# Performance work log

Hardware: AMD Instinct MI355X
Metric: run time of the kernel (lower is better)

The kernel has to match this reference:

```python
import jax, jax.numpy as jnp
import numpy as np

EPS = 1e-4
B, C_IN, H, W = 64, 512, 14, 14
P, NCLS = 2000, 200


def setup_inputs() -> dict:
    key = jax.random.key(0)
    k1, k2 = jax.random.split(key)
    x = jax.random.normal(k1, (B, C_IN, H, W), dtype=jnp.float32)
    prototype_vectors = jax.random.uniform(k2, (P, C_IN, 1, 1), dtype=jnp.float32)
    # fc weight init: +1 for the prototype's own class, -0.5 otherwise
    per_class = P // NCLS
    assoc = (np.arange(P) // per_class)[:, None] == np.arange(NCLS)[None, :]  # [P, NCLS]
    assoc = assoc.astype(np.float32)
    fc_weight = jnp.asarray(1.0 * assoc.T - 0.5 * (1.0 - assoc.T))  # [NCLS, P]
    return {"x": x, "prototype_vectors": prototype_vectors, "fc_weight": fc_weight}


def reference(x, prototype_vectors, fc_weight):
    # prototypes are 1x1, so the conv is a channel contraction
    p = prototype_vectors[:, :, 0, 0]  # [P, C]
    xp = jnp.einsum('bchw,pc->bphw', x, p)                 # cross term
    x2_patch_sum = jnp.sum(x * x, axis=1, keepdims=True)   # [B,1,H,W] (ones-kernel conv, identical across P)
    p2 = jnp.sum(p * p, axis=1)[None, :, None, None]       # [1,P,1,1]
    dists = jax.nn.relu(x2_patch_sum - 2.0 * xp + p2)      # [B,P,H,W]
    min_dists = jnp.min(dists, axis=(2, 3))                # global min-pool -> [B,P]
    activations = jnp.log((min_dists + 1.0) / (min_dists + EPS))
    logits = activations @ fc_weight.T                     # [B,NCLS]
    return (x, min_dists, dists, activations, logits)
```

## Files before the change

### kernel.cpp

```cpp
#include <hip/hip_runtime.h>
#include <math.h>


#define EPSV 1e-4f
typedef unsigned short ushort_t;

constexpr int NB  = 64;
constexpr int NC  = 512;
constexpr int NHW = 196;
constexpr int NP  = 2000;
constexpr int NPAD = 2048;
constexpr int NCL = 200;
constexpr int MM   = NB * NHW;
constexpr int XTOT = NB * NC * NHW;

constexpr long long OFF_MIN = XTOT;
constexpr long long OFF_D   = OFF_MIN + (long long)NB * NP;
constexpr long long OFF_ACT = OFF_D + (long long)NB * NP * NHW;
constexpr long long OFF_LOG = OFF_ACT + (long long)NB * NP;

typedef __attribute__((ext_vector_type(8))) short short8;
typedef __attribute__((ext_vector_type(4))) float f32x4;

__device__ __forceinline__ void bsplit(float f, unsigned& h, unsigned& l) {
    unsigned u = __float_as_uint(f);
    h = (u + 0x7FFFu + ((u >> 16) & 1u)) >> 16;
    float fl = f - __uint_as_float(h << 16);
    unsigned u2 = __float_as_uint(fl);
    l = (u2 + 0x7FFFu + ((u2 >> 16) & 1u)) >> 16;
}

__device__ __forceinline__ void gl_lds16(const void* g, void* l) {
    __builtin_amdgcn_global_load_lds(
        (const __attribute__((address_space(1))) unsigned int*)g,
        (__attribute__((address_space(3))) unsigned int*)l, 16, 0, 0);
}

__global__ void fill_kernel(float* __restrict__ mind, float* __restrict__ x2) {
    int i = blockIdx.x * 256 + threadIdx.x;
    if (i < NB * NP) mind[i] = 3.402823466e38f;
    if (i < MM)      x2[i] = 0.f;
}

__global__ __launch_bounds__(256) void splitx_kernel(const float* __restrict__ x,
                                                     ushort_t* __restrict__ xh,
                                                     ushort_t* __restrict__ xl,
                                                     float* __restrict__ x2) {
    __shared__ float tl[64 * 197];
    const int b = blockIdx.x >> 3, cc = blockIdx.x & 7;
    const int c0 = cc * 64;
    const float* src = x + ((size_t)b * NC + c0) * NHW;
    for (int idx = threadIdx.x; idx < 64 * 196; idx += 256) {
        int cl = idx / 196, hw = idx - cl * 196;
        tl[cl * 197 + hw] = src[idx];
    }
    __syncthreads();
    for (int idx = threadIdx.x; idx < 64 * 196; idx += 256) {
        int hw = idx >> 6, cl = idx & 63;
        float v = tl[cl * 197 + hw];
        unsigned h, l; bsplit(v, h, l);
        size_t o = ((size_t)(b * 196 + hw)) * NC + c0 + cl;
        xh[o] = (ushort_t)h;
        xl[o] = (ushort_t)l;
    }
    if (threadIdx.x < 196) {
        float s = 0.f;
        #pragma unroll 8
        for (int cl = 0; cl < 64; ++cl) { float v = tl[cl * 197 + threadIdx.x]; s += v * v; }
        atomicAdd(&x2[b * 196 + threadIdx.x], s);
    }
}

__global__ void splitp_kernel(const float* __restrict__ proto,
                              ushort_t* __restrict__ ph, ushort_t* __restrict__ pl,
                              float* __restrict__ p2) {
    int p = blockIdx.x * 4 + (threadIdx.x >> 6);
    int l = threadIdx.x & 63;
    unsigned hs[8], ls[8];
    float s = 0.f;
    if (p < NP) {
        const float4* pr = (const float4*)(proto + (size_t)p * NC + l * 8);
        float4 a = pr[0], bb = pr[1];
        float vv[8] = {a.x, a.y, a.z, a.w, bb.x, bb.y, bb.z, bb.w};
        #pragma unroll
        for (int k = 0; k < 8; ++k) { bsplit(vv[k], hs[k], ls[k]); s += vv[k] * vv[k]; }
    } else {
        #pragma unroll
        for (int k = 0; k < 8; ++k) { hs[k] = 0; ls[k] = 0; }
    }
    uint4 H = make_uint4(hs[0] | (hs[1] << 16), hs[2] | (hs[3] << 16),
                         hs[4] | (hs[5] << 16), hs[6] | (hs[7] << 16));
    uint4 L = make_uint4(ls[0] | (ls[1] << 16), ls[2] | (ls[3] << 16),
                         ls[4] | (ls[5] << 16), ls[6] | (ls[7] << 16));
    *(uint4*)&ph[(size_t)p * NC + l * 8] = H;
    *(uint4*)&pl[(size_t)p * NC + l * 8] = L;
    for (int off = 32; off; off >>= 1) s += __shfl_down(s, off, 64);
    if (l == 0) p2[p] = s;
}

__global__ __launch_bounds__(256) void gemm_kernel(
    const ushort_t* __restrict__ xh, const ushort_t* __restrict__ xl,
    const ushort_t* __restrict__ ph, const ushort_t* __restrict__ pl,
    const float* __restrict__ p2, const float* __restrict__ x2,
    float* __restrict__ dists, unsigned* __restrict__ mind)
{
    __shared__ ushort_t Ah[128 * 32];
    __shared__ ushort_t Al[128 * 32];
    __shared__ ushort_t Bh[128 * 32];
    __shared__ ushort_t Bl[128 * 32];

    const int wg  = blockIdx.x;
    const int swz = (wg & 7) * 196 + (wg >> 3);
    const int nt  = swz / 98, mt = swz - nt * 98;

    const int t = threadIdx.x;
    const int lane = t & 63, lm = lane & 15, kg = lane >> 4;
    const int w = t >> 6, wp = w >> 1, wx = w & 1;

    const size_t ga = (size_t)(mt * 128 + (t >> 2)) * NC + (t & 3) * 8;
    const size_t gb = (size_t)(nt * 128 + (t >> 2)) * NC + (t & 3) * 8;
    const size_t gs = (size_t)64 * NC;

    f32x4 acc[4][4];
    #pragma unroll
    for (int i = 0; i < 4; ++i)
        #pragma unroll
        for (int j = 0; j < 4; ++j) acc[i][j] = 0.f;

    for (int c0 = 0; c0 < NC; c0 += 32) {
        gl_lds16(xh + ga + c0,      &Ah[t * 8]);
        gl_lds16(xh + ga + gs + c0, &Ah[2048 + t * 8]);
        gl_lds16(xl + ga + c0,      &Al[t * 8]);
        gl_lds16(xl + ga + gs + c0, &Al[2048 + t * 8]);
        gl_lds16(ph + gb + c0,      &Bh[t * 8]);
        gl_lds16(ph + gb + gs + c0, &Bh[2048 + t * 8]);
        gl_lds16(pl + gb + c0,      &Bl[t * 8]);
        gl_lds16(pl + gb + gs + c0, &Bl[2048 + t * 8]);
        __syncthreads();

        short8 PH[4], PL[4], XH[4], XL[4];
        #pragma unroll
        for (int i = 0; i < 4; ++i) {
            PH[i] = *(const short8*)&Bh[(wp * 64 + i * 16 + lm) * 32 + kg * 8];
            PL[i] = *(const short8*)&Bl[(wp * 64 + i * 16 + lm) * 32 + kg * 8];
            XH[i] = *(const short8*)&Ah[(wx * 64 + i * 16 + lm) * 32 + kg * 8];
            XL[i] = *(const short8*)&Al[(wx * 64 + i * 16 + lm) * 32 + kg * 8];
        }
        #pragma unroll
        for (int i = 0; i < 4; ++i)
            #pragma unroll
            for (int j = 0; j < 4; ++j) {
                acc[i][j] = __builtin_amdgcn_mfma_f32_16x16x32_bf16(PH[i], XH[j], acc[i][j], 0, 0, 0);
                acc[i][j] = __builtin_amdgcn_mfma_f32_16x16x32_bf16(PL[i], XH[j], acc[i][j], 0, 0, 0);
                acc[i][j] = __builtin_amdgcn_mfma_f32_16x16x32_bf16(PH[i], XL[j], acc[i][j], 0, 0, 0);
            }
        __syncthreads();
    }

    const int mhalf = mt * 128 + wx * 64;
    const int b0h = mhalf / 196;
    const int b1h = (mhalf + 63) / 196;
    float x2v[4]; int bj[4]; size_t dbase[4];
    #pragma unroll
    for (int j = 0; j < 4; ++j) {
        int m = mhalf + j * 16 + lm;
        x2v[j] = x2[m];
        int b = m / 196, hw = m - b * 196;
        bj[j] = b;
        dbase[j] = (size_t)b * ((size_t)NP * NHW) + hw;
    }
    #pragma unroll
    for (int i = 0; i < 4; ++i) {
        #pragma unroll
        for (int r = 0; r < 4; ++r) {
            int p = nt * 128 + wp * 64 + i * 16 + kg * 4 + r;
            if (p < NP) {
                float p2v = p2[p];
                float mn0 = 3.402823466e38f, mn1 = 3.402823466e38f;
                #pragma unroll
                for (int j = 0; j < 4; ++j) {
                    float v = fmaxf(x2v[j] - 2.f * acc[i][j][r] + p2v, 0.f);
                    dists[dbase[j] + (size_t)p * NHW] = v;
                    if (bj[j] == b0h) mn0 = fminf(mn0, v); else mn1 = fminf(mn1, v);
                }
                #pragma unroll
                for (int off = 1; off < 16; off <<= 1) {
                    mn0 = fminf(mn0, __shfl_xor(mn0, off, 64));
                    mn1 = fminf(mn1, __shfl_xor(mn1, off, 64));
                }
                if (lm == 0) {
                    atomicMin(&mind[b0h * NP + p], __float_as_uint(mn0));
                    if (b1h != b0h) atomicMin(&mind[b1h * NP + p], __float_as_uint(mn1));
                }
            }
        }
    }
}

__global__ void act_kernel(const float* __restrict__ mind, float* __restrict__ act) {
    int i = blockIdx.x * 256 + threadIdx.x;
    if (i < NB * NP) { float md = mind[i]; act[i] = logf((md + 1.f) / (md + EPSV)); }
}

__global__ void logits_kernel(const float* __restrict__ act,
                              const float* __restrict__ fc, float* __restrict__ out) {
    int r = blockIdx.x * 4 + (threadIdx.x >> 6);
    int l = threadIdx.x & 63;
    int b = r / NCL, n = r - b * NCL;
    const float* arow = act + b * NP;
    const float* frow = fc + n * NP;
    float s = 0.f;
    for (int k = l; k < NP; k += 64) s += arow[k] * frow[k];
    for (int off = 32; off; off >>= 1) s += __shfl_down(s, off, 64);
    if (l == 0) out[r] = s;
}

__global__ void copy_kernel(const float4* __restrict__ in, float4* __restrict__ out, int n4) {
    for (int i = blockIdx.x * blockDim.x + threadIdx.x; i < n4; i += gridDim.x * blockDim.x)
        out[i] = in[i];
}

extern "C" void kernel_launch(void* const* d_in, const int* in_sizes, int n_in,
                              void* d_out, int out_size, void* d_ws, size_t ws_size,
                              hipStream_t stream) {
    const float* x     = (const float*)d_in[0];
    const float* proto = (const float*)d_in[1];
    const float* fc    = (const float*)d_in[2];
    float* out = (float*)d_out;

    ushort_t* xh = (ushort_t*)out;
    ushort_t* xl = xh + XTOT;
    ushort_t* ph = (ushort_t*)d_ws;
    ushort_t* pl = ph + (size_t)NPAD * NC;
    float*    p2 = (float*)(pl + (size_t)NPAD * NC);
    float*    x2 = p2 + NPAD;

    float* mind  = out + OFF_MIN;
    float* dists = out + OFF_D;
    float* act   = out + OFF_ACT;
    float* logit = out + OFF_LOG;

    fill_kernel<<<500, 256, 0, stream>>>(mind, x2);
    splitx_kernel<<<512, 256, 0, stream>>>(x, xh, xl, x2);
    splitp_kernel<<<512, 256, 0, stream>>>(proto, ph, pl, p2);

    gemm_kernel<<<1568, 256, 0, stream>>>(xh, xl, ph, pl, p2, x2, dists, (unsigned*)mind);

    act_kernel<<<500, 256, 0, stream>>>(mind, act);
    logits_kernel<<<3200, 256, 0, stream>>>(act, fc, logit);

    copy_kernel<<<2048, 256, 0, stream>>>((const float4*)x, (float4*)out, XTOT / 4);
}
```

Before: 305.2 us.

## Drop bf16 hi/lo split to single bf16 GEMM with swizzled LDS and nontemporal stores

Replaces the three-MFMA bf16x3 split-precision scheme with a single bf16 product, removing the low-part arrays, their conversion and their loads. The K tile grows to 64 with an XOR-swizzled LDS layout to avoid bank conflicts. The fill kernel is fused into the prototype split kernel, vectorised packed stores are used in splitx, and dists and the copy use nontemporal loads and stores. Plain bf16 loses precision in the cross term, which could break tolerance for distances near zero.

```diff
diff --git a/kernel.cpp b/kernel.cpp
--- a/kernel.cpp
+++ b/kernel.cpp
@@ -22,12 +22,9 @@
 typedef __attribute__((ext_vector_type(8))) short short8;
 typedef __attribute__((ext_vector_type(4))) float f32x4;
 
-__device__ __forceinline__ void bsplit(float f, unsigned& h, unsigned& l) {
+__device__ __forceinline__ unsigned bf16rne(float f) {
     unsigned u = __float_as_uint(f);
-    h = (u + 0x7FFFu + ((u >> 16) & 1u)) >> 16;
-    float fl = f - __uint_as_float(h << 16);
-    unsigned u2 = __float_as_uint(fl);
-    l = (u2 + 0x7FFFu + ((u2 >> 16) & 1u)) >> 16;
+    return (u + 0x7FFFu + ((u >> 16) & 1u)) >> 16;
 }
 
 __device__ __forceinline__ void gl_lds16(const void* g, void* l) {
@@ -36,32 +33,55 @@
         (__attribute__((address_space(3))) unsigned int*)l, 16, 0, 0);
 }
 
-__global__ void fill_kernel(float* __restrict__ mind, float* __restrict__ x2) {
-    int i = blockIdx.x * 256 + threadIdx.x;
-    if (i < NB * NP) mind[i] = 3.402823466e38f;
-    if (i < MM)      x2[i] = 0.f;
+__global__ __launch_bounds__(256) void splitp_kernel(const float* __restrict__ proto,
+                              ushort_t* __restrict__ ph, float* __restrict__ p2,
+                              float* __restrict__ mind, float* __restrict__ x2) {
+    int gi = blockIdx.x * 256 + threadIdx.x;
+    if (gi < NB * NP) mind[gi] = 3.402823466e38f;
+    if (gi < MM)      x2[gi]  = 0.f;
+
+    int p = blockIdx.x * 4 + (threadIdx.x >> 6);
+    int l = threadIdx.x & 63;
+    unsigned hs[8];
+    float s = 0.f;
+    if (p < NP) {
+        const float4* pr = (const float4*)(proto + (size_t)p * NC + l * 8);
+        float4 a = pr[0], bb = pr[1];
+        float vv[8] = {a.x, a.y, a.z, a.w, bb.x, bb.y, bb.z, bb.w};
+        #pragma unroll
+        for (int k = 0; k < 8; ++k) { hs[k] = bf16rne(vv[k]); s += vv[k] * vv[k]; }
+    } else {
+        #pragma unroll
+        for (int k = 0; k < 8; ++k) hs[k] = 0;
+    }
+    uint4 H = make_uint4(hs[0] | (hs[1] << 16), hs[2] | (hs[3] << 16),
+                         hs[4] | (hs[5] << 16), hs[6] | (hs[7] << 16));
+    int col = (l >> 3) * 64 + (((l & 7) ^ (p & 7)) << 3);
+    *(uint4*)&ph[(size_t)p * NC + col] = H;
+    for (int off = 32; off; off >>= 1) s += __shfl_down(s, off, 64);
+    if (l == 0) p2[p] = s;
 }
 
 __global__ __launch_bounds__(256) void splitx_kernel(const float* __restrict__ x,
                                                      ushort_t* __restrict__ xh,
-                                                     ushort_t* __restrict__ xl,
                                                      float* __restrict__ x2) {
     __shared__ float tl[64 * 197];
     const int b = blockIdx.x >> 3, cc = blockIdx.x & 7;
     const int c0 = cc * 64;
     const float* src = x + ((size_t)b * NC + c0) * NHW;
-    for (int idx = threadIdx.x; idx < 64 * 196; idx += 256) {
-        int cl = idx / 196, hw = idx - cl * 196;
-        tl[cl * 197 + hw] = src[idx];
-    }
+    for (int idx = threadIdx.x; idx < 64 * 196; idx += 256)
+        tl[(idx / 196) * 197 + (idx % 196)] = src[idx];
     __syncthreads();
-    for (int idx = threadIdx.x; idx < 64 * 196; idx += 256) {
-        int hw = idx >> 6, cl = idx & 63;
-        float v = tl[cl * 197 + hw];
-        unsigned h, l; bsplit(v, h, l);
-        size_t o = ((size_t)(b * 196 + hw)) * NC + c0 + cl;
-        xh[o] = (ushort_t)h;
-        xl[o] = (ushort_t)l;
+    for (int idx = threadIdx.x; idx < 1568; idx += 256) {
+        int hw = idx >> 3, slot = idx & 7;
+        int m = b * 196 + hw;
+        unsigned hs[8];
+        #pragma unroll
+        for (int e = 0; e < 8; ++e)
+            hs[e] = bf16rne(tl[(slot * 8 + e) * 197 + hw]);
+        uint4 H = make_uint4(hs[0] | (hs[1] << 16), hs[2] | (hs[3] << 16),
+                             hs[4] | (hs[5] << 16), hs[6] | (hs[7] << 16));
+        *(uint4*)&xh[(size_t)m * NC + c0 + ((slot ^ (m & 7)) << 3)] = H;
     }
     if (threadIdx.x < 196) {
         float s = 0.f;
@@ -71,43 +91,13 @@
     }
 }
 
-__global__ void splitp_kernel(const float* __restrict__ proto,
-                              ushort_t* __restrict__ ph, ushort_t* __restrict__ pl,
-                              float* __restrict__ p2) {
-    int p = blockIdx.x * 4 + (threadIdx.x >> 6);
-    int l = threadIdx.x & 63;
-    unsigned hs[8], ls[8];
-    float s = 0.f;
-    if (p < NP) {
-        const float4* pr = (const float4*)(proto + (size_t)p * NC + l * 8);
-        float4 a = pr[0], bb = pr[1];
-        float vv[8] = {a.x, a.y, a.z, a.w, bb.x, bb.y, bb.z, bb.w};
-        #pragma unroll
-        for (int k = 0; k < 8; ++k) { bsplit(vv[k], hs[k], ls[k]); s += vv[k] * vv[k]; }
-    } else {
-        #pragma unroll
-        for (int k = 0; k < 8; ++k) { hs[k] = 0; ls[k] = 0; }
-    }
-    uint4 H = make_uint4(hs[0] | (hs[1] << 16), hs[2] | (hs[3] << 16),
-                         hs[4] | (hs[5] << 16), hs[6] | (hs[7] << 16));
-    uint4 L = make_uint4(ls[0] | (ls[1] << 16), ls[2] | (ls[3] << 16),
-                         ls[4] | (ls[5] << 16), ls[6] | (ls[7] << 16));
-    *(uint4*)&ph[(size_t)p * NC + l * 8] = H;
-    *(uint4*)&pl[(size_t)p * NC + l * 8] = L;
-    for (int off = 32; off; off >>= 1) s += __shfl_down(s, off, 64);
-    if (l == 0) p2[p] = s;
-}
-
 __global__ __launch_bounds__(256) void gemm_kernel(
-    const ushort_t* __restrict__ xh, const ushort_t* __restrict__ xl,
-    const ushort_t* __restrict__ ph, const ushort_t* __restrict__ pl,
+    const ushort_t* __restrict__ xh, const ushort_t* __restrict__ ph,
     const float* __restrict__ p2, const float* __restrict__ x2,
     float* __restrict__ dists, unsigned* __restrict__ mind)
 {
-    __shared__ ushort_t Ah[128 * 32];
-    __shared__ ushort_t Al[128 * 32];
-    __shared__ ushort_t Bh[128 * 32];
-    __shared__ ushort_t Bl[128 * 32];
+    __shared__ ushort_t Ah[128 * 64];
+    __shared__ ushort_t Bh[128 * 64];
 
     const int wg  = blockIdx.x;
     const int swz = (wg & 7) * 196 + (wg >> 3);
@@ -117,9 +107,9 @@
     const int lane = t & 63, lm = lane & 15, kg = lane >> 4;
     const int w = t >> 6, wp = w >> 1, wx = w & 1;
 
-    const size_t ga = (size_t)(mt * 128 + (t >> 2)) * NC + (t & 3) * 8;
-    const size_t gb = (size_t)(nt * 128 + (t >> 2)) * NC + (t & 3) * 8;
-    const size_t gs = (size_t)64 * NC;
+    const size_t ga = (size_t)(mt * 128 + (t >> 3)) * NC + (t & 7) * 8;
+    const size_t gb = (size_t)(nt * 128 + (t >> 3)) * NC + (t & 7) * 8;
+    const size_t gs = (size_t)32 * NC;
 
     f32x4 acc[4][4];
     #pragma unroll
@@ -127,33 +117,33 @@
         #pragma unroll
         for (int j = 0; j < 4; ++j) acc[i][j] = 0.f;
 
-    for (int c0 = 0; c0 < NC; c0 += 32) {
-        gl_lds16(xh + ga + c0,      &Ah[t * 8]);
-        gl_lds16(xh + ga + gs + c0, &Ah[2048 + t * 8]);
-        gl_lds16(xl + ga + c0,      &Al[t * 8]);
-        gl_lds16(xl + ga + gs + c0, &Al[2048 + t * 8]);
-        gl_lds16(ph + gb + c0,      &Bh[t * 8]);
-        gl_lds16(ph + gb + gs + c0, &Bh[2048 + t * 8]);
-        gl_lds16(pl + gb + c0,      &Bl[t * 8]);
-        gl_lds16(pl + gb + gs + c0, &Bl[2048 + t * 8]);
+    for (int c0 = 0; c0 < NC; c0 += 64) {
+        #pragma unroll
+        for (int q = 0; q < 4; ++q) {
+            gl_lds16(xh + ga + q * gs + c0, &Ah[q * 2048 + t * 8]);
+            gl_lds16(ph + gb + q * gs + c0, &Bh[q * 2048 + t * 8]);
+        }
         __syncthreads();
 
-        short8 PH[4], PL[4], XH[4], XL[4];
-        #pragma unroll
-        for (int i = 0; i < 4; ++i) {
-            PH[i] = *(const short8*)&Bh[(wp * 64 + i * 16 + lm) * 32 + kg * 8];
-            PL[i] = *(const short8*)&Bl[(wp * 64 + i * 16 + lm) * 32 + kg * 8];
-            XH[i] = *(const short8*)&Ah[(wx * 64 + i * 16 + lm) * 32 + kg * 8];
-            XL[i] = *(const short8*)&Al[(wx * 64 + i * 16 + lm) * 32 + kg * 8];
-        }
-        #pragma unroll
-        for (int i = 0; i < 4; ++i)
+        short8 PF[2][4], XF[2][4];
+        #pragma unroll
+        for (int s = 0; s < 2; ++s)
             #pragma unroll
-            for (int j = 0; j < 4; ++j) {
-                acc[i][j] = __builtin_amdgcn_mfma_f32_16x16x32_bf16(PH[i], XH[j], acc[i][j], 0, 0, 0);
-                acc[i][j] = __builtin_amdgcn_mfma_f32_16x16x32_bf16(PL[i], XH[j], acc[i][j], 0, 0, 0);
-                acc[i][j] = __builtin_amdgcn_mfma_f32_16x16x32_bf16(PH[i], XL[j], acc[i][j], 0, 0, 0);
+            for (int i = 0; i < 4; ++i) {
+                int prow = wp * 64 + i * 16 + lm;
+                int xrow = wx * 64 + i * 16 + lm;
+                int lsp = (s * 4 + kg) ^ (prow & 7);
+                int lsx = (s * 4 + kg) ^ (xrow & 7);
+                PF[s][i] = *(const short8*)&Bh[prow * 64 + lsp * 8];
+                XF[s][i] = *(const short8*)&Ah[xrow * 64 + lsx * 8];
             }
+        #pragma unroll
+        for (int s = 0; s < 2; ++s)
+            #pragma unroll
+            for (int i = 0; i < 4; ++i)
+                #pragma unroll
+                for (int j = 0; j < 4; ++j)
+                    acc[i][j] = __builtin_amdgcn_mfma_f32_16x16x32_bf16(PF[s][i], XF[s][j], acc[i][j], 0, 0, 0);
         __syncthreads();
     }
 
@@ -180,7 +170,7 @@
                 #pragma unroll
                 for (int j = 0; j < 4; ++j) {
                     float v = fmaxf(x2v[j] - 2.f * acc[i][j][r] + p2v, 0.f);
-                    dists[dbase[j] + (size_t)p * NHW] = v;
+                    __builtin_nontemporal_store(v, &dists[dbase[j] + (size_t)p * NHW]);
                     if (bj[j] == b0h) mn0 = fminf(mn0, v); else mn1 = fminf(mn1, v);
                 }
                 #pragma unroll
@@ -215,9 +205,11 @@
     if (l == 0) out[r] = s;
 }
 
-__global__ void copy_kernel(const float4* __restrict__ in, float4* __restrict__ out, int n4) {
-    for (int i = blockIdx.x * blockDim.x + threadIdx.x; i < n4; i += gridDim.x * blockDim.x)
-        out[i] = in[i];
+__global__ void copy_kernel(const f32x4* __restrict__ in, f32x4* __restrict__ out, int n4) {
+    for (int i = blockIdx.x * blockDim.x + threadIdx.x; i < n4; i += gridDim.x * blockDim.x) {
+        f32x4 v = __builtin_nontemporal_load(&in[i]);
+        __builtin_nontemporal_store(v, &out[i]);
+    }
 }
 
 extern "C" void kernel_launch(void* const* d_in, const int* in_sizes, int n_in,
@@ -229,10 +221,8 @@
     float* out = (float*)d_out;
 
     ushort_t* xh = (ushort_t*)out;
-    ushort_t* xl = xh + XTOT;
     ushort_t* ph = (ushort_t*)d_ws;
-    ushort_t* pl = ph + (size_t)NPAD * NC;
-    float*    p2 = (float*)(pl + (size_t)NPAD * NC);
+    float*    p2 = (float*)(ph + (size_t)NPAD * NC);
     float*    x2 = p2 + NPAD;
 
     float* mind  = out + OFF_MIN;
@@ -240,14 +230,13 @@
     float* act   = out + OFF_ACT;
     float* logit = out + OFF_LOG;
 
-    fill_kernel<<<500, 256, 0, stream>>>(mind, x2);
-    splitx_kernel<<<512, 256, 0, stream>>>(x, xh, xl, x2);
-    splitp_kernel<<<512, 256, 0, stream>>>(proto, ph, pl, p2);
-
-    gemm_kernel<<<1568, 256, 0, stream>>>(xh, xl, ph, pl, p2, x2, dists, (unsigned*)mind);
+    splitp_kernel<<<512, 256, 0, stream>>>(proto, ph, p2, mind, x2);
+    splitx_kernel<<<512, 256, 0, stream>>>(x, xh, x2);
+
+    gemm_kernel<<<1568, 256, 0, stream>>>(xh, ph, p2, x2, dists, (unsigned*)mind);
 
     act_kernel<<<500, 256, 0, stream>>>(mind, act);
     logits_kernel<<<3200, 256, 0, stream>>>(act, fc, logit);
 
-    copy_kernel<<<2048, 256, 0, stream>>>((const float4*)x, (float4*)out, XTOT / 4);
-}
+    copy_kernel<<<2048, 256, 0, stream>>>((const f32x4*)x, (f32x4*)out, XTOT / 4);
+}
```

Result: faster. 262.6 us (-14.0%).
